# Optimization experiments

Measured on AMD Instinct MI355X. Metric: run time of the kernel, lower is better.

The kernel has to match this reference:

```python
import jax, jax.numpy as jnp
import numpy as np
from jax import lax

K = 3  # deformable kernel size


def conv2d(x, w, b):
    # x: [B,C,H,W], w: [O,I,kh,kw], 'SAME' padding, stride 1
    out = lax.conv_general_dilated(x, w, (1, 1), 'SAME',
                                   dimension_numbers=('NCHW', 'OIHW', 'NCHW'))
    return out + b[None, :, None, None]


def deform_conv2d(x, dy, dx, mask, dw, db):
    # Deformable conv v2 (torchvision semantics): bilinear sample at
    # p0 + p_k + delta_p_k, zero outside, modulated by sigmoid mask.
    # x:[B,C,H,W]  dy,dx,mask:[B,H,W,K2]  dw:[O,C,K,K]  db:[O]
    B, C, H, W = x.shape
    K2 = K * K
    pad = K // 2
    ky = (jnp.arange(K2) // K).astype(x.dtype) - pad  # kernel row offsets
    kx = (jnp.arange(K2) % K).astype(x.dtype) - pad
    hy = jnp.arange(H, dtype=x.dtype)[:, None, None]
    wx = jnp.arange(W, dtype=x.dtype)[None, :, None]
    py = hy + ky[None, None, :] + dy  # [B,H,W,K2] sample rows
    px = wx + kx[None, None, :] + dx  # [B,H,W,K2] sample cols

    xf = x.reshape(B, C, H * W)
    gat = jax.vmap(lambda xfb, idx: xfb[:, idx])  # -> [B,C,H,W,K2]

    y0 = jnp.floor(py)
    x0 = jnp.floor(px)
    samp = jnp.zeros((B, C, H, W, K2), x.dtype)
    # accumulate the 4 bilinear corners (zero padding outside image)
    for yc, wy in ((y0, y0 + 1.0 - py), (y0 + 1.0, py - y0)):
        for xc, wxx in ((x0, x0 + 1.0 - px), (x0 + 1.0, px - x0)):
            valid = (yc >= 0) & (yc < H) & (xc >= 0) & (xc < W)
            idx = (jnp.clip(yc, 0, H - 1) * W
                   + jnp.clip(xc, 0, W - 1)).astype(jnp.int32)
            wgt = jnp.where(valid, wy * wxx, jnp.zeros((), x.dtype))
            samp = samp + gat(xf, idx) * wgt[:, None]  # [B,C,H,W,K2]

    samp = samp * mask[:, None]  # modulation: [B,1,H,W,K2]
    out = jnp.einsum('bchwk,ock->bohw', samp, dw.reshape(dw.shape[0], C, K2))
    return out + db[None, :, None, None]


def setup_inputs() -> dict:
    key = jax.random.key(0)
    ks = jax.random.split(key, 8)
    B, C, H, W = 8, 64, 128, 128
    K2 = K * K
    x = jax.random.normal(ks[0], (B, C, H, W), jnp.float32)
    # offset conv (3x3) -> 2*K2 channels; small init so offsets are modest
    ow = 0.02 * jax.random.normal(ks[1], (2 * K2, C, 3, 3), jnp.float32)
    ob = jnp.zeros((2 * K2,), jnp.float32)
    # mask conv (3x3) -> K2 channels
    mw = 0.02 * jax.random.normal(ks[2], (K2, C, 3, 3), jnp.float32)
    mb = jnp.zeros((K2,), jnp.float32)
    # deformable conv weights (C->C, KxK)
    dw = (1.0 / np.sqrt(C * K2)) * jax.random.normal(ks[3], (C, C, K, K), jnp.float32)
    db = jnp.zeros((C,), jnp.float32)
    return {'x': x, 'ow': ow, 'ob': ob, 'mw': mw, 'mb': mb, 'dw': dw, 'db': db}


def reference(x, ow, ob, mw, mb, dw, db):
    B, C, H, W = x.shape
    K2 = K * K
    offset = conv2d(x, ow, ob)                    # [B,2K2,H,W]
    mask = jax.nn.sigmoid(conv2d(x, mw, mb))      # [B,K2,H,W]
    off = offset.reshape(B, K2, 2, H, W)
    dy = off[:, :, 0].transpose(0, 2, 3, 1)       # [B,H,W,K2] (torchvision: even=dy)
    dx = off[:, :, 1].transpose(0, 2, 3, 1)
    return deform_conv2d(x, dy, dx, mask.transpose(0, 2, 3, 1), dw, db)
```

## Files before the change

### kernel.cpp

```cpp
#include <hip/hip_runtime.h>

#define BATCH 8
#define CIN   64
#define HW    16384
#define CK    576

typedef __attribute__((ext_vector_type(8))) short bf16x8;
typedef __attribute__((ext_vector_type(4))) float f32x4;
typedef __attribute__((ext_vector_type(2))) float f32x2;

__device__ inline unsigned short f2bf(float f) {
    unsigned int u = __builtin_bit_cast(unsigned int, f);
    u += 0x7FFFu + ((u >> 16) & 1u);
    return (unsigned short)(u >> 16);
}
__device__ inline float bf2f(unsigned short u) {
    return __builtin_bit_cast(float, (unsigned)u << 16);
}
__device__ inline f32x2 upk2(unsigned u) {
    f32x2 r;
    r[0] = __builtin_bit_cast(float, u << 16);
    r[1] = __builtin_bit_cast(float, u & 0xFFFF0000u);
    return r;
}
__device__ inline unsigned pk2bf(f32x2 s) {
    return (unsigned)f2bf(s[0]) | ((unsigned)f2bf(s[1]) << 16);
}


__global__ __launch_bounds__(256) void prep_transpose(
        const float* __restrict__ x, const float* __restrict__ ow,
        const float* __restrict__ mw, const float* __restrict__ dw,
        unsigned short* __restrict__ wpack, unsigned short* __restrict__ wcpack,
        unsigned short* __restrict__ xT) {
    int t = threadIdx.x, blk = blockIdx.x;
    {
        int b = blk & 7, r2 = blk >> 3;
        int h = r2 >> 1, hf = r2 & 1;
        int gx = (hf << 6) + (t & 63);
        int w = t >> 6;
        int pix = (h << 7) + gx;
        const float* __restrict__ xb = x + (b * CIN) * HW + pix;
        bf16x8 lo, hi;
#pragma unroll
        for (int i = 0; i < 8; i++) lo[i] = (short)f2bf(xb[(w * 16 + i) * HW]);
#pragma unroll
        for (int i = 0; i < 8; i++) hi[i] = (short)f2bf(xb[(w * 16 + 8 + i) * HW]);
        unsigned short* dst = xT + ((b * HW + pix) << 6) + w * 16;
        *(bf16x8*)dst = lo;
        *(bf16x8*)(dst + 8) = hi;
    }
    int g = blk * 256 + t;
    if (g < 18 * 4 * 64 * 8) {
        int j = g & 7, lane = (g >> 3) & 63, ot = (g >> 9) & 3, gks = g >> 11;
        int o = ot * 16 + (lane & 15);
        int s = gks * 32 + ((lane >> 4) & 3) * 8 + j;
        int c = s & 63, tap = s >> 6;
        wpack[g] = f2bf(dw[o * CK + c * 9 + tap]);
    }
    if (g < 18 * 2 * 64 * 8) {
        int j = g & 7, lane = (g >> 3) & 63, ot = (g >> 9) & 1, gks = g >> 10;
        int o = ot * 16 + (lane & 15);
        int s = gks * 32 + ((lane >> 4) & 3) * 8 + j;
        int c = s & 63, tap = s >> 6;
        float v = 0.f;
        if (o < 18)      v = ow[(o * 64 + c) * 9 + tap];
        else if (o < 27) v = mw[((o - 18) * 64 + c) * 9 + tap];
        wcpack[g] = f2bf(v);
    }
}

__global__ __launch_bounds__(256, 3) void fused_kernel(
        const unsigned short* __restrict__ xT, const unsigned short* __restrict__ wcpack,
        const unsigned short* __restrict__ wpack,
        const float* __restrict__ ob, const float* __restrict__ mb,
        const float* __restrict__ dbv, float* __restrict__ out) {
    __shared__ unsigned short buf[18560];
    __shared__ unsigned short omrow[2048];
    __shared__ int ptab[576];

    int t = threadIdx.x;
    int lane = t & 63, pt = t >> 6, quad = lane >> 4, n = lane & 15;
    int blk = blockIdx.x;
    int b = blk & 7, r2 = blk >> 3;
    int h = r2 >> 1, hf = r2 & 1;
    int px0 = hf << 6;
    int pxl = (pt << 4) + n;
    int gx  = px0 + pxl;

    const unsigned short* __restrict__ xtb = xT + ((b * HW) << 6);
    const short zs = 0;
    const bf16x8 zv = {zs, zs, zs, zs, zs, zs, zs, zs};

    for (int i = t; i < 1584; i += 256) {
        int s  = i & 7;
        int rc = i >> 3;
        int r  = rc / 66, col = rc - r * 66;
        int gy  = h - 1 + r;
        int gxc = px0 - 1 + col;
        bf16x8 v = zv;
        if ((unsigned)gy < 128u && (unsigned)gxc < 128u)
            v = *(const bf16x8*)(xtb + (((gy << 7) + gxc) << 6) + (s << 3));
        *(bf16x8*)&buf[rc * 72 + (s << 3)] = v;
    }
    __syncthreads();

    {
        f32x4 acc0 = {0.f, 0.f, 0.f, 0.f}, acc1 = {0.f, 0.f, 0.f, 0.f};
#pragma unroll
        for (int tap = 0; tap < 9; tap++) {
            int r = tap / 3, cm = tap % 3;
            const unsigned short* srcA = &buf[(r * 66 + pxl + cm) * 72];
#pragma unroll
            for (int kk = 0; kk < 2; kk++) {
                bf16x8 bfrag = *(const bf16x8*)(srcA + (kk << 5) + (quad << 3));
                int gks = tap * 2 + kk;
                bf16x8 a0 = *(const bf16x8*)(wcpack + ((gks * 2 + 0) * 64 + lane) * 8);
                bf16x8 a1 = *(const bf16x8*)(wcpack + ((gks * 2 + 1) * 64 + lane) * 8);
                acc0 = __builtin_amdgcn_mfma_f32_16x16x32_bf16(a0, bfrag, acc0, 0, 0, 0);
                acc1 = __builtin_amdgcn_mfma_f32_16x16x32_bf16(a1, bfrag, acc1, 0, 0, 0);
            }
        }
        {
            unsigned short p[4];
#pragma unroll
            for (int r = 0; r < 4; r++) p[r] = f2bf(acc0[r] + ob[quad * 4 + r]);
            uint2 u;
            u.x = (unsigned)p[0] | ((unsigned)p[1] << 16);
            u.y = (unsigned)p[2] | ((unsigned)p[3] << 16);
            *(uint2*)&omrow[pxl * 32 + quad * 4] = u;
        }
        {
            unsigned short p[4];
#pragma unroll
            for (int r = 0; r < 4; r++) {
                int o = 16 + quad * 4 + r;
                float v = acc1[r];
                if (o < 18) v += ob[o];
                else if (o < 27) { v += mb[o - 18]; v = 1.f / (1.f + __expf(-v)); }
                else v = 0.f;
                p[r] = f2bf(v);
            }
            uint2 u;
            u.x = (unsigned)p[0] | ((unsigned)p[1] << 16);
            u.y = (unsigned)p[2] | ((unsigned)p[3] << 16);
            *(uint2*)&omrow[pxl * 32 + 16 + quad * 4] = u;
        }
    }
    __syncthreads();

    float w00[9], w01[9], w10[9], w11[9];
#pragma unroll
    for (int k = 0; k < 9; k++) {
        float dy = bf2f(omrow[pxl * 32 + 2 * k]);
        float dx = bf2f(omrow[pxl * 32 + 2 * k + 1]);
        float mk = bf2f(omrow[pxl * 32 + 18 + k]);
        float py  = (float)h  + (float)(k / 3 - 1) + dy;
        float pxx = (float)gx + (float)(k % 3 - 1) + dx;
        float fy = floorf(py), fx = floorf(pxx);
        float ly = py - fy, lx = pxx - fx;
        int y0 = (int)fy, x0 = (int)fx;
        bool y0v = (unsigned)y0 < 128u, y1v = (unsigned)(y0 + 1) < 128u;
        bool x0v = (unsigned)x0 < 128u, x1v = (unsigned)(x0 + 1) < 128u;
        w00[k] = (y0v && x0v) ? (1.f - ly) * (1.f - lx) * mk : 0.f;
        w01[k] = (y0v && x1v) ? (1.f - ly) * lx * mk : 0.f;
        w10[k] = (y1v && x0v) ? ly * (1.f - lx) * mk : 0.f;
        w11[k] = (y1v && x1v) ? ly * lx * mk : 0.f;
        int y0c = min(max(y0, 0), 127), x0c = min(max(x0, 0), 127);
        int dxb = (x0 >= 0 && x0 < 127) ? 1 : 0;
        int dyb = (y0 >= 0 && y0 < 127) ? 1 : 0;
        if (quad == 0)
            ptab[pxl * 9 + k] = ((y0c << 7) + x0c) | (dxb << 14) | (dyb << 15);
    }
    __syncthreads();

    f32x4 acc[4];
#pragma unroll
    for (int ot = 0; ot < 4; ot++) acc[ot] = (f32x4){0.f, 0.f, 0.f, 0.f};

    unsigned short* gbw = &buf[(pt << 2) * 1160];

#pragma unroll
    for (int tap = 0; tap < 9; tap++) {
#pragma unroll
        for (int i = 0; i < 8; i++) {
            int m = lane + (i << 6);
            int s = m & 7, c = (m >> 3) & 3, pxn = (m >> 5) & 15;
            int p = ptab[((pt << 4) + pxn) * 9 + tap];
            int base = p & 0x3FFF;
            int dxb  = (p >> 14) & 1;
            int dyo  = ((p >> 15) & 1) << 7;
            int row = base + ((-(c & 1)) & dxb) + ((-((c >> 1) & 1)) & dyo);
            bf16x8 v = *(const bf16x8*)(xtb + (row << 6) + (s << 3));
            *(bf16x8*)&gbw[c * 1160 + pxn * 72 + (s << 3)] = v;
        }
        f32x2 W0 = {w00[tap], w00[tap]}, W1 = {w01[tap], w01[tap]};
        f32x2 W2 = {w10[tap], w10[tap]}, W3 = {w11[tap], w11[tap]};
        const unsigned short* gbr = &gbw[n * 72];
#pragma unroll
        for (int kk = 0; kk < 2; kk++) {
            int co = (kk << 5) + (quad << 3);
            bf16x8 v00 = *(const bf16x8*)(gbr + 0 * 1160 + co);
            bf16x8 v01 = *(const bf16x8*)(gbr + 1 * 1160 + co);
            bf16x8 v10 = *(const bf16x8*)(gbr + 2 * 1160 + co);
            bf16x8 v11 = *(const bf16x8*)(gbr + 3 * 1160 + co);
            const unsigned* u00 = (const unsigned*)&v00;
            const unsigned* u01 = (const unsigned*)&v01;
            const unsigned* u10 = (const unsigned*)&v10;
            const unsigned* u11 = (const unsigned*)&v11;
            bf16x8 bfrag;
            unsigned* bu = (unsigned*)&bfrag;
#pragma unroll
            for (int jj = 0; jj < 4; jj++) {
                f32x2 s2 = upk2(u00[jj]) * W0 + upk2(u01[jj]) * W1
                         + upk2(u10[jj]) * W2 + upk2(u11[jj]) * W3;
                bu[jj] = pk2bf(s2);
            }
            int gks = tap * 2 + kk;
#pragma unroll
            for (int ot = 0; ot < 4; ot++) {
                bf16x8 af = *(const bf16x8*)(wpack + ((gks * 4 + ot) * 64 + lane) * 8);
                acc[ot] = __builtin_amdgcn_mfma_f32_16x16x32_bf16(af, bfrag, acc[ot], 0, 0, 0);
            }
        }
    }

    int opix = (h << 7) + px0 + (pt << 4) + n;
#pragma unroll
    for (int ot = 0; ot < 4; ot++) {
#pragma unroll
        for (int r = 0; r < 4; r++) {
            int o = ot * 16 + quad * 4 + r;
            out[(b * 64 + o) * HW + opix] = acc[ot][r] + dbv[o];
        }
    }
}

extern "C" void kernel_launch(void* const* d_in, const int* in_sizes, int n_in,
                              void* d_out, int out_size, void* d_ws, size_t ws_size,
                              hipStream_t stream) {
    const float* x   = (const float*)d_in[0];
    const float* ow  = (const float*)d_in[1];
    const float* ob  = (const float*)d_in[2];
    const float* mw  = (const float*)d_in[3];
    const float* mb  = (const float*)d_in[4];
    const float* dw  = (const float*)d_in[5];
    const float* dbv = (const float*)d_in[6];
    float* out = (float*)d_out;

    unsigned short* wpack  = (unsigned short*)d_ws;
    unsigned short* wcpack = wpack + 36864;
    unsigned short* xT     = wpack + 55296;

    prep_transpose<<<2048, 256, 0, stream>>>(x, ow, mw, dw, wpack, wcpack, xT);
    fused_kernel<<<2048, 256, 0, stream>>>(xT, wcpack, wpack, ob, mb, dbv, out);
}
```

Before: 164.8 us.

## Prefetch next tap's gathered corners into registers; move bilinear weights to LDS

```diff
diff --git a/kernel.cpp b/kernel.cpp
--- a/kernel.cpp
+++ b/kernel.cpp
@@ -78,6 +78,7 @@
     __shared__ unsigned short buf[18560];
     __shared__ unsigned short omrow[2048];
     __shared__ int ptab[576];
+    __shared__ float wtab[2304];
 
     int t = threadIdx.x;
     int lane = t & 63, pt = t >> 6, quad = lane >> 4, n = lane & 15;
@@ -149,7 +150,6 @@
     }
     __syncthreads();
 
-    float w00[9], w01[9], w10[9], w11[9];
 #pragma unroll
     for (int k = 0; k < 9; k++) {
         float dy = bf2f(omrow[pxl * 32 + 2 * k]);
@@ -162,15 +162,18 @@
         int y0 = (int)fy, x0 = (int)fx;
         bool y0v = (unsigned)y0 < 128u, y1v = (unsigned)(y0 + 1) < 128u;
         bool x0v = (unsigned)x0 < 128u, x1v = (unsigned)(x0 + 1) < 128u;
-        w00[k] = (y0v && x0v) ? (1.f - ly) * (1.f - lx) * mk : 0.f;
-        w01[k] = (y0v && x1v) ? (1.f - ly) * lx * mk : 0.f;
-        w10[k] = (y1v && x0v) ? ly * (1.f - lx) * mk : 0.f;
-        w11[k] = (y1v && x1v) ? ly * lx * mk : 0.f;
+        f32x4 wv;
+        wv[0] = (y0v && x0v) ? (1.f - ly) * (1.f - lx) * mk : 0.f;
+        wv[1] = (y0v && x1v) ? (1.f - ly) * lx * mk : 0.f;
+        wv[2] = (y1v && x0v) ? ly * (1.f - lx) * mk : 0.f;
+        wv[3] = (y1v && x1v) ? ly * lx * mk : 0.f;
         int y0c = min(max(y0, 0), 127), x0c = min(max(x0, 0), 127);
         int dxb = (x0 >= 0 && x0 < 127) ? 1 : 0;
         int dyb = (y0 >= 0 && y0 < 127) ? 1 : 0;
-        if (quad == 0)
+        if (quad == 0) {
             ptab[pxl * 9 + k] = ((y0c << 7) + x0c) | (dxb << 14) | (dyb << 15);
+            *(f32x4*)&wtab[(pxl * 9 + k) * 4] = wv;
+        }
     }
     __syncthreads();
 
@@ -179,23 +182,41 @@
     for (int ot = 0; ot < 4; ot++) acc[ot] = (f32x4){0.f, 0.f, 0.f, 0.f};
 
     unsigned short* gbw = &buf[(pt << 2) * 1160];
+    int soff   = (lane & 7) << 3;
+    int c2     = (lane >> 3) & 3;
+    int cm1    = -(c2 & 1);
+    int cm2    = -((c2 >> 1) & 1);
+    int pxnb   = lane >> 5;
+    int pibase = (pt << 4) * 9;
+    int gwbase = c2 * 1160 + soff;
+    int setbase = pxl * 9;
+
+    bf16x8 pf[8];
+#pragma unroll
+    for (int i = 0; i < 8; i++) {
+        int p = ptab[pibase + (pxnb + 2 * i) * 9];
+        int row = (p & 0x3FFF) + (cm1 & ((p >> 14) & 1)) + (cm2 & (((p >> 15) & 1) << 7));
+        pf[i] = *(const bf16x8*)(xtb + (row << 6) + soff);
+    }
 
 #pragma unroll
     for (int tap = 0; tap < 9; tap++) {
-#pragma unroll
-        for (int i = 0; i < 8; i++) {
-            int m = lane + (i << 6);
-            int s = m & 7, c = (m >> 3) & 3, pxn = (m >> 5) & 15;
-            int p = ptab[((pt << 4) + pxn) * 9 + tap];
-            int base = p & 0x3FFF;
-            int dxb  = (p >> 14) & 1;
-            int dyo  = ((p >> 15) & 1) << 7;
-            int row = base + ((-(c & 1)) & dxb) + ((-((c >> 1) & 1)) & dyo);
-            bf16x8 v = *(const bf16x8*)(xtb + (row << 6) + (s << 3));
-            *(bf16x8*)&gbw[c * 1160 + pxn * 72 + (s << 3)] = v;
-        }
-        f32x2 W0 = {w00[tap], w00[tap]}, W1 = {w01[tap], w01[tap]};
-        f32x2 W2 = {w10[tap], w10[tap]}, W3 = {w11[tap], w11[tap]};
+        bf16x8 nf[8];
+        if (tap < 8) {
+#pragma unroll
+            for (int i = 0; i < 8; i++) {
+                int p = ptab[pibase + (pxnb + 2 * i) * 9 + tap + 1];
+                int row = (p & 0x3FFF) + (cm1 & ((p >> 14) & 1)) + (cm2 & (((p >> 15) & 1) << 7));
+                nf[i] = *(const bf16x8*)(xtb + (row << 6) + soff);
+            }
+        }
+#pragma unroll
+        for (int i = 0; i < 8; i++)
+            *(bf16x8*)&gbw[gwbase + (pxnb + 2 * i) * 72] = pf[i];
+
+        f32x4 wv = *(const f32x4*)&wtab[(setbase + tap) * 4];
+        f32x2 W0 = {wv[0], wv[0]}, W1 = {wv[1], wv[1]};
+        f32x2 W2 = {wv[2], wv[2]}, W3 = {wv[3], wv[3]};
         const unsigned short* gbr = &gbw[n * 72];
 #pragma unroll
         for (int kk = 0; kk < 2; kk++) {
@@ -223,6 +244,10 @@
                 acc[ot] = __builtin_amdgcn_mfma_f32_16x16x32_bf16(af, bfrag, acc[ot], 0, 0, 0);
             }
         }
+        if (tap < 8) {
+#pragma unroll
+            for (int i = 0; i < 8; i++) pf[i] = nf[i];
+        }
     }
 
     int opix = (h << 7) + px0 + (pt << 4) + n;
```

Result: faster. 160.1 us (-2.9%).

## Gather bilinear corners directly from global into registers, drop LDS staging

Applied to the files above, without the earlier changes.

```diff
diff --git a/kernel.cpp b/kernel.cpp
--- a/kernel.cpp
+++ b/kernel.cpp
@@ -75,9 +75,8 @@
         const unsigned short* __restrict__ wpack,
         const float* __restrict__ ob, const float* __restrict__ mb,
         const float* __restrict__ dbv, float* __restrict__ out) {
-    __shared__ unsigned short buf[18560];
+    __shared__ unsigned short buf[14256];
     __shared__ unsigned short omrow[2048];
-    __shared__ int ptab[576];
 
     int t = threadIdx.x;
     int lane = t & 63, pt = t >> 6, quad = lane >> 4, n = lane & 15;
@@ -150,6 +149,7 @@
     __syncthreads();
 
     float w00[9], w01[9], w10[9], w11[9];
+    int pk[9];
 #pragma unroll
     for (int k = 0; k < 9; k++) {
         float dy = bf2f(omrow[pxl * 32 + 2 * k]);
@@ -169,41 +169,32 @@
         int y0c = min(max(y0, 0), 127), x0c = min(max(x0, 0), 127);
         int dxb = (x0 >= 0 && x0 < 127) ? 1 : 0;
         int dyb = (y0 >= 0 && y0 < 127) ? 1 : 0;
-        if (quad == 0)
-            ptab[pxl * 9 + k] = ((y0c << 7) + x0c) | (dxb << 14) | (dyb << 15);
-    }
-    __syncthreads();
+        pk[k] = ((y0c << 7) + x0c) | (dxb << 14) | (dyb << 15);
+    }
 
     f32x4 acc[4];
 #pragma unroll
     for (int ot = 0; ot < 4; ot++) acc[ot] = (f32x4){0.f, 0.f, 0.f, 0.f};
 
-    unsigned short* gbw = &buf[(pt << 2) * 1160];
-
 #pragma unroll
     for (int tap = 0; tap < 9; tap++) {
-#pragma unroll
-        for (int i = 0; i < 8; i++) {
-            int m = lane + (i << 6);
-            int s = m & 7, c = (m >> 3) & 3, pxn = (m >> 5) & 15;
-            int p = ptab[((pt << 4) + pxn) * 9 + tap];
-            int base = p & 0x3FFF;
-            int dxb  = (p >> 14) & 1;
-            int dyo  = ((p >> 15) & 1) << 7;
-            int row = base + ((-(c & 1)) & dxb) + ((-((c >> 1) & 1)) & dyo);
-            bf16x8 v = *(const bf16x8*)(xtb + (row << 6) + (s << 3));
-            *(bf16x8*)&gbw[c * 1160 + pxn * 72 + (s << 3)] = v;
-        }
+        int p = pk[tap];
+        int base = p & 0x3FFF;
+        int dxb  = (p >> 14) & 1;
+        int dyo  = ((p >> 15) & 1) << 7;
+        const unsigned short* __restrict__ r00 = xtb + (base << 6);
+        const unsigned short* __restrict__ r01 = xtb + ((base + dxb) << 6);
+        const unsigned short* __restrict__ r10 = xtb + ((base + dyo) << 6);
+        const unsigned short* __restrict__ r11 = xtb + ((base + dyo + dxb) << 6);
         f32x2 W0 = {w00[tap], w00[tap]}, W1 = {w01[tap], w01[tap]};
         f32x2 W2 = {w10[tap], w10[tap]}, W3 = {w11[tap], w11[tap]};
-        const unsigned short* gbr = &gbw[n * 72];
 #pragma unroll
         for (int kk = 0; kk < 2; kk++) {
             int co = (kk << 5) + (quad << 3);
-            bf16x8 v00 = *(const bf16x8*)(gbr + 0 * 1160 + co);
-            bf16x8 v01 = *(const bf16x8*)(gbr + 1 * 1160 + co);
-            bf16x8 v10 = *(const bf16x8*)(gbr + 2 * 1160 + co);
-            bf16x8 v11 = *(const bf16x8*)(gbr + 3 * 1160 + co);
+            bf16x8 v00 = *(const bf16x8*)(r00 + co);
+            bf16x8 v01 = *(const bf16x8*)(r01 + co);
+            bf16x8 v10 = *(const bf16x8*)(r10 + co);
+            bf16x8 v11 = *(const bf16x8*)(r11 + co);
             const unsigned* u00 = (const unsigned*)&v00;
             const unsigned* u01 = (const unsigned*)&v01;
             const unsigned* u10 = (const unsigned*)&v10;
```

Measured after the change: 191.5 us. 1.16x slower.
